# Kernel tuning notes

Hardware: AMD Instinct MI355X
Metric: run time of the kernel (lower is better)

The kernel has to match this reference:

```python
import jax, jax.numpy as jnp
import numpy as np

# ---- static config (matches init_kwargs) ----
B = 8            # batch_size (graphs)
N = 10000        # num_nodes per graph
NTOT = B * N     # total node rows (80000)
E = 320000       # edges (only over first N nodes, as in the original code)
D = 128          # input_dim == backbone_channels (shared conv forces equality)
H = 4            # heads
C = 128          # backbone_channels (per-head out dim, concat=False)
L = 3            # num_backbone_layers
K = 30           # sort-pool k
HID = 512        # mlp_hidden_dim
OUT = 2          # output_dim
EXPECTED = K * L * C * H + 1  # buggy mlp_input_dim from __init__ -> zero-pad
BN_EPS = 1e-5


def setup_inputs() -> dict:
    key = jax.random.key(0)
    ks = jax.random.split(key, 20)
    s = 1.0 / np.sqrt(D)
    inp = {
        "x": jax.random.normal(ks[0], (NTOT, D), dtype=jnp.float32),
        "edge_index": jax.random.randint(ks[1], (2, E), 0, N, dtype=jnp.int32),
        "age": jax.random.normal(ks[2], (B,), dtype=jnp.float32),
        # shared TransformerConv params (reused across all L layers)
        "Wq": jax.random.normal(ks[3], (D, H * C), dtype=jnp.float32) * s,
        "bq": jax.random.normal(ks[4], (H * C,), dtype=jnp.float32) * 0.02,
        "Wk": jax.random.normal(ks[5], (D, H * C), dtype=jnp.float32) * s,
        "bk": jax.random.normal(ks[6], (H * C,), dtype=jnp.float32) * 0.02,
        "Wv": jax.random.normal(ks[7], (D, H * C), dtype=jnp.float32) * s,
        "bv": jax.random.normal(ks[8], (H * C,), dtype=jnp.float32) * 0.02,
        "Wskip": jax.random.normal(ks[9], (D, C), dtype=jnp.float32) * s,
        "bskip": jax.random.normal(ks[10], (C,), dtype=jnp.float32) * 0.02,
        # per-layer BatchNorm (eval mode: running stats)
        "bn_gamma": 1.0 + 0.1 * jax.random.normal(ks[11], (L, C), dtype=jnp.float32),
        "bn_beta": 0.1 * jax.random.normal(ks[12], (L, C), dtype=jnp.float32),
        "bn_mean": 0.1 * jax.random.normal(ks[13], (L, C), dtype=jnp.float32),
        "bn_var": jax.random.uniform(ks[14], (L, C), dtype=jnp.float32, minval=0.5, maxval=1.5),
        # MLP head (2 layers: EXPECTED->HID, ReLU, HID->OUT)
        "W1": jax.random.normal(ks[15], (EXPECTED, HID), dtype=jnp.float32) * (1.0 / np.sqrt(EXPECTED)),
        "b1": jnp.zeros((HID,), dtype=jnp.float32),
        "W2": jax.random.normal(ks[16], (HID, OUT), dtype=jnp.float32) * (1.0 / np.sqrt(HID)),
        "b2": jnp.zeros((OUT,), dtype=jnp.float32),
    }
    return inp


def _transformer_conv(h, src, dst, Wq, bq, Wk, bk, Wv, bv, Wskip, bskip):
    # PyG TransformerConv, concat=False, root_weight=True, eval (no attn dropout)
    q = (h @ Wq + bq).reshape(NTOT, H, C)
    k = (h @ Wk + bk).reshape(NTOT, H, C)
    v = (h @ Wv + bv).reshape(NTOT, H, C)
    # per-edge attention logits [E, H]
    alpha = jnp.einsum("ehc,ehc->eh", q[dst], k[src]) / np.sqrt(C).astype(np.float32)
    # segment softmax over incoming edges of each target node
    m = jax.ops.segment_max(alpha, dst, num_segments=NTOT)          # [NTOT, H]
    e = jnp.exp(alpha - m[dst])
    denom = jax.ops.segment_sum(e, dst, num_segments=NTOT)          # [NTOT, H]
    a = e / (denom[dst] + 1e-16)                                    # [E, H]
    out = jax.ops.segment_sum(a[:, :, None] * v[src], dst, num_segments=NTOT)  # [NTOT,H,C]
    return out.mean(axis=1) + h @ Wskip + bskip                     # concat=False -> head mean


def reference(x, edge_index, age, Wq, bq, Wk, bk, Wv, bv, Wskip, bskip,
              bn_gamma, bn_beta, bn_mean, bn_var, W1, b1, W2, b2):
    src, dst = edge_index[0], edge_index[1]
    h = x
    feats = []
    for i in range(L):  # fixed small layer count; shared conv weights
        h = _transformer_conv(h, src, dst, Wq, bq, Wk, bk, Wv, bv, Wskip, bskip)
        h = (h - bn_mean[i]) * (bn_gamma[i] / jnp.sqrt(bn_var[i] + BN_EPS)) + bn_beta[i]
        h = jax.nn.relu(h)  # dropout: eval mode no-op
        feats.append(h)
    h = feats[-1]  # concat_input_graph=False
    # global_sort_pool: sort nodes per graph by last channel (desc), take top-k
    xr = h.reshape(B, N, C)
    idx = jnp.argsort(-xr[:, :, -1], axis=1)[:, :K]                 # [B, K]
    pooled = jnp.take_along_axis(xr, idx[:, :, None], axis=1)       # [B, K, C]
    z = pooled.reshape(B, K * C)
    z = jnp.concatenate([z, age.reshape(B, 1)], axis=1)             # [B, K*C+1]
    # zero-pad to the (mismatched) expected MLP input dim, as in the original
    z = jnp.concatenate([z, jnp.zeros((B, EXPECTED - z.shape[1]), dtype=z.dtype)], axis=1)
    z = jax.nn.relu(z @ W1 + b1)
    z = z @ W2 + b2
    return jax.nn.log_softmax(z, axis=-1)
```

## Files before the change

### kernel.cpp

```cpp
#include <hip/hip_runtime.h>
#include <cmath>


#define NN    10000
#define NTOT  80000
#define EE    320000
#define CH    128

__device__ __forceinline__ float rl_f(float v, int lane) {
    return __uint_as_float(__builtin_amdgcn_readlane(__float_as_uint(v), lane));
}

__global__ __launch_bounds__(256) void precompute_kernel(
    const float* __restrict__ Wq, const float* __restrict__ bq,
    const float* __restrict__ Wk, const float* __restrict__ Wv,
    const float* __restrict__ bv, const float* __restrict__ Wskip,
    const float* __restrict__ bskip,
    const float* __restrict__ bn_gamma, const float* __restrict__ bn_beta,
    const float* __restrict__ bn_mean, const float* __restrict__ bn_var,
    float* __restrict__ Bcat, float* __restrict__ biascat,
    float* __restrict__ Wcomb, float* __restrict__ bvbar,
    float* __restrict__ bnS, float* __restrict__ bnB)
{
    const float inv_sqrtC = 0.08838834764831845f;
    int idx = blockIdx.x * 256 + threadIdx.x;
    if (idx < 65536) {
        int c = idx >> 9;
        int o = idx & 511;
        int hbase = o & ~127;
        int j = o & 127;
        const float* wq = Wq + c * 512 + hbase;
        const float* wk = Wk + j * 512 + hbase;
        float s = 0.f;
        for (int cc = 0; cc < 128; cc++) s = fmaf(wq[cc], wk[cc], s);
        Bcat[c * 640 + o] = s * inv_sqrtC;
        return;
    }
    idx -= 65536;
    if (idx < 16384) {
        int c = idx >> 7, n = idx & 127;
        Bcat[c * 640 + 512 + n] = Wskip[c * 128 + n];
        return;
    }
    idx -= 16384;
    if (idx < 512) {
        int o = idx, hbase = o & ~127, j = o & 127;
        const float* wk = Wk + j * 512 + hbase;
        const float* bqp = bq + hbase;
        float s = 0.f;
        for (int cc = 0; cc < 128; cc++) s = fmaf(bqp[cc], wk[cc], s);
        biascat[o] = s * inv_sqrtC;
        return;
    }
    idx -= 512;
    if (idx < 128) {
        biascat[512 + idx] = bskip[idx];
        return;
    }
    idx -= 128;
    if (idx < 65536) {
        int k = idx >> 7;
        int n = idx & 127;
        int h = k >> 7, c = k & 127;
        Wcomb[k * 128 + n] = Wv[c * 512 + h * 128 + n] * 0.25f;
        return;
    }
    idx -= 65536;
    if (idx < 128) {
        float s = 0.f;
        for (int h = 0; h < 4; h++) s += bv[h * 128 + idx];
        bvbar[idx] = 0.25f * s;
        return;
    }
    idx -= 128;
    if (idx < 384) {
        float sc = bn_gamma[idx] / sqrtf(bn_var[idx] + 1e-5f);
        bnS[idx] = sc;
        bnB[idx] = bn_beta[idx] - bn_mean[idx] * sc;
        return;
    }
}

__global__ void count_kernel(const int* __restrict__ dst, int* __restrict__ deg) {
    int e = blockIdx.x * 256 + threadIdx.x;
    if (e < EE) atomicAdd(&deg[dst[e]], 1);
}

__global__ __launch_bounds__(1024) void scan_kernel(const int* __restrict__ deg,
                                                    int* __restrict__ rowstart) {
    __shared__ int part[1024];
    const int t = threadIdx.x;
    int loc[10];
    int s = 0;
    for (int i = 0; i < 10; i++) {
        int idx = t * 10 + i;
        int v = (idx < NN) ? deg[idx] : 0;
        loc[i] = s; s += v;
    }
    part[t] = s; __syncthreads();
    for (int d = 1; d < 1024; d <<= 1) {
        int v = (t >= d) ? part[t - d] : 0;
        __syncthreads();
        part[t] += v;
        __syncthreads();
    }
    int base = (t == 0) ? 0 : part[t - 1];
    for (int i = 0; i < 10; i++) {
        int idx = t * 10 + i;
        if (idx <= NN) rowstart[idx] = base + loc[i];
    }
}

__global__ void scatter_kernel(const int* __restrict__ src, const int* __restrict__ dst,
                               const int* __restrict__ rowstart, int* __restrict__ cursor,
                               int* __restrict__ csr_src) {
    int e = blockIdx.x * 256 + threadIdx.x;
    if (e < EE) {
        int d = dst[e];
        int p = atomicAdd(&cursor[d], 1);
        csr_src[rowstart[d] + p] = src[e];
    }
}

__global__ __launch_bounds__(256, 4) void skip_keys_kernel(
    const float* __restrict__ xup,
    const float* __restrict__ Wskip,
    const float* __restrict__ bskip,
    const float* __restrict__ bnS, const float* __restrict__ bnB,
    float* __restrict__ gkeys)
{
    __shared__ float rowb[64][132];
    __shared__ float sWc[128];
    const int t = threadIdx.x;
    const int l = t & 63;
    const int wv = __builtin_amdgcn_readfirstlane(t >> 6);
    const int colbase = wv * 32;
    const int r0 = blockIdx.x * 64;
    const int Mrem = min(64, (NTOT - NN) - r0);

    for (int f = t; f < 64 * 32; f += 256) {
        int row = f >> 5, c4 = (f & 31) * 4;
        float4 v = make_float4(0.f, 0.f, 0.f, 0.f);
        if (row < Mrem) v = *(const float4*)(xup + (size_t)(r0 + row) * CH + c4);
        *(float4*)&rowb[row][c4] = v;
    }
    if (t < 128) sWc[t] = Wskip[t * 128 + 127];
    __syncthreads();

    for (int layer = 0; layer < 2; layer++) {
        float acc[32];
        #pragma unroll
        for (int c = 0; c < 32; c++) acc[c] = 0.f;
        const float* Wb = Wskip + colbase;
        for (int kq = 0; kq < 32; kq++) {
            const float4 a4 = *(const float4*)&rowb[l][kq * 4];
            #pragma unroll
            for (int q = 0; q < 4; q++) {
                const float av = (q == 0) ? a4.x : (q == 1) ? a4.y
                               : (q == 2) ? a4.z : a4.w;
                const float* wr = Wb + (kq * 4 + q) * 128;
                #pragma unroll
                for (int c = 0; c < 32; c++)
                    acc[c] = fmaf(av, wr[c], acc[c]);
            }
        }
        __syncthreads();
        const float* bS = bnS + layer * 128;
        const float* bB = bnB + layer * 128;
        #pragma unroll
        for (int c4 = 0; c4 < 8; c4++) {
            float4 v;
            float* vp = &v.x;
            #pragma unroll
            for (int q = 0; q < 4; q++) {
                const int n = colbase + c4 * 4 + q;
                float xv = acc[c4 * 4 + q] + bskip[n];
                xv = fmaf(xv, bS[n], bB[n]);
                vp[q] = fmaxf(xv, 0.f);
            }
            *(float4*)&rowb[l][colbase + c4 * 4] = v;
        }
        __syncthreads();
    }
    if (t < Mrem) {
        float s = 0.f;
        for (int k = 0; k < 128; k++) s = fmaf(rowb[t][k], sWc[k], s);
        s += bskip[127];
        s = fmaf(s, bnS[2 * 128 + 127], bnB[2 * 128 + 127]);
        gkeys[NN + r0 + t] = fmaxf(s, 0.f);
    }
}

template<int BM, int BN, int TM, int TN, int MODE>
__global__ __launch_bounds__(256) void gemm_fp32(
    const float* __restrict__ A, int lda,
    const float* __restrict__ B, int ldb,
    const float* __restrict__ bias, const float* __restrict__ bias2,
    const int* __restrict__ deg,
    const float* __restrict__ Cold,
    const float* __restrict__ bnS, const float* __restrict__ bnB,
    float* __restrict__ C0, int ldc0,
    float* __restrict__ C1, int ldc1,
    int M, int K,
    float* __restrict__ keysOut)
{
    constexpr int BK = 16;
    __shared__ float As[BK][BM + 4];
    __shared__ float Bs[BK][BN + 4];
    const int t  = threadIdx.x;
    const int tx = t % (BN / TN);
    const int ty = t / (BN / TN);
    const int m0 = blockIdx.x * BM;
    const int n0 = blockIdx.y * BN;
    float acc[TM][TN];
    #pragma unroll
    for (int i = 0; i < TM; i++)
        #pragma unroll
        for (int j = 0; j < TN; j++) acc[i][j] = 0.f;

    for (int k0 = 0; k0 < K; k0 += BK) {
        #pragma unroll
        for (int f = t; f < BM * 4; f += 256) {
            int row = f >> 2, fc = f & 3;
            int gm = m0 + row;
            float4 v = make_float4(0.f, 0.f, 0.f, 0.f);
            if (gm < M) v = *(const float4*)(A + (size_t)gm * lda + k0 + fc * 4);
            As[fc * 4 + 0][row] = v.x;
            As[fc * 4 + 1][row] = v.y;
            As[fc * 4 + 2][row] = v.z;
            As[fc * 4 + 3][row] = v.w;
        }
        #pragma unroll
        for (int f = t; f < BK * (BN / 4); f += 256) {
            int kk = f / (BN / 4);
            int nn = (f % (BN / 4)) * 4;
            *(float4*)(&Bs[kk][nn]) = *(const float4*)(B + (size_t)(k0 + kk) * ldb + n0 + nn);
        }
        __syncthreads();
        #pragma unroll
        for (int kk = 0; kk < BK; kk++) {
            float af[TM], bf[TN];
            if constexpr (TM == 2) {
                float2 v = *(const float2*)&As[kk][ty * 2];
                af[0] = v.x; af[1] = v.y;
            } else {
                float4 v = *(const float4*)&As[kk][ty * 4];
                af[0] = v.x; af[1] = v.y; af[2] = v.z; af[3] = v.w;
            }
            if constexpr (TN == 4) {
                float4 v = *(const float4*)&Bs[kk][tx * 4];
                bf[0] = v.x; bf[1] = v.y; bf[2] = v.z; bf[3] = v.w;
            } else {
                float4 v = *(const float4*)&Bs[kk][tx * 4];
                float4 w = *(const float4*)&Bs[kk][BN / 2 + tx * 4];
                bf[0] = v.x; bf[1] = v.y; bf[2] = v.z; bf[3] = v.w;
                bf[4] = w.x; bf[5] = w.y; bf[6] = w.z; bf[7] = w.w;
            }
            #pragma unroll
            for (int i = 0; i < TM; i++)
                #pragma unroll
                for (int j = 0; j < TN; j++)
                    acc[i][j] = fmaf(af[i], bf[j], acc[i][j]);
        }
        __syncthreads();
    }
    #pragma unroll
    for (int i = 0; i < TM; i++) {
        const int gm = m0 + ty * TM + i;
        if (gm >= M) continue;
        const bool addB2 = (MODE == 4) ? (deg[gm] > 0) : false;
        #pragma unroll
        for (int h = 0; h < TN / 4; h++) {
            const int nb = n0 + ((TN == 8) ? h * (BN / 2) + tx * 4 : tx * TN + h * 4);
            float4 v;
            float* vp = &v.x;
            if (MODE == 4) {
                const float4 old = *(const float4*)(Cold + (size_t)gm * ldc1 + nb);
                const float* op = &old.x;
                #pragma unroll
                for (int q = 0; q < 4; q++) {
                    const int n = nb + q;
                    float x = acc[i][h * 4 + q] + op[q];
                    if (addB2) x += bias2[n];
                    x = fmaf(x, bnS[n], bnB[n]);
                    vp[q] = fmaxf(x, 0.f);
                }
                *(float4*)(C0 + (size_t)gm * ldc0 + nb) = v;
                if (keysOut != nullptr && nb == 124) keysOut[gm] = v.w;
            } else {
                #pragma unroll
                for (int q = 0; q < 4; q++)
                    vp[q] = acc[i][h * 4 + q] + bias[nb + q];
                if (nb < 512)
                    *(float4*)(C0 + (size_t)gm * ldc0 + nb) = v;
                else
                    *(float4*)(C1 + (size_t)gm * ldc1 + nb - 512) = v;
            }
        }
    }
}

__global__ __launch_bounds__(256) void attn_kernel(
    const float* __restrict__ h,
    const float* __restrict__ u,
    float* __restrict__ g,
    const int* __restrict__ rowstart,
    const int* __restrict__ csr_src)
{
    __shared__ float h_lds[128 * 65];
    __shared__ __align__(16) float palpha[4 * 64 * 4];
    __shared__ __align__(16) float wT[64 * 4];
    __shared__ __align__(16) float scale_lds[4];
    __shared__ __align__(16) float s_lds[4];
    __shared__ __align__(16) float merge[128 * 4];
    __shared__ int src_lds[64];

    const int n  = blockIdx.x;
    const int t  = threadIdx.x;
    const int w  = t >> 6;
    const int l  = t & 63;
    const int c  = t & 127;
    const int jh = t >> 7;
    const int rs   = rowstart[n];
    const int degn = rowstart[n + 1] - rs;

    if (degn == 0) {
        g[(size_t)n * 512 + t] = 0.f;
        g[(size_t)n * 512 + 256 + t] = 0.f;
        return;
    }
    float u_reg0 = u[(size_t)n * 512 + ((l >> 5)) * 128 + 32 * w + (l & 31)];
    float u_reg1 = u[(size_t)n * 512 + ((l >> 5) + 2) * 128 + 32 * w + (l & 31)];

    float m_run = -INFINITY, s_run = 0.f;
    float4 acc4 = make_float4(0.f, 0.f, 0.f, 0.f);

    for (int base = 0; base < degn; base += 64) {
        const int len = min(64, degn - base);
        __syncthreads();
        if (t < len) src_lds[t] = csr_src[rs + base + t];
        __syncthreads();
        for (int f = t; f < len * 32; f += 256) {
            const int j = f >> 5, c4 = (f & 31) * 4;
            const float4 v = *(const float4*)(h + (size_t)src_lds[j] * CH + c4);
            h_lds[(c4 + 0) * 65 + j] = v.x;
            h_lds[(c4 + 1) * 65 + j] = v.y;
            h_lds[(c4 + 2) * 65 + j] = v.z;
            h_lds[(c4 + 3) * 65 + j] = v.w;
        }
        __syncthreads();
        {
            float p0 = 0.f, p1 = 0.f, p2 = 0.f, p3 = 0.f;
            #pragma unroll
            for (int dc = 0; dc < 32; dc++) {
                const float hv = h_lds[(32 * w + dc) * 65 + l];
                p0 = fmaf(rl_f(u_reg0, dc),      hv, p0);
                p1 = fmaf(rl_f(u_reg0, 32 + dc), hv, p1);
                p2 = fmaf(rl_f(u_reg1, dc),      hv, p2);
                p3 = fmaf(rl_f(u_reg1, 32 + dc), hv, p3);
            }
            palpha[(0 * 64 + l) * 4 + w] = p0;
            palpha[(1 * 64 + l) * 4 + w] = p1;
            palpha[(2 * 64 + l) * 4 + w] = p2;
            palpha[(3 * 64 + l) * 4 + w] = p3;
        }
        __syncthreads();
        {
            const float4 pa = *(const float4*)&palpha[(w * 64 + l) * 4];
            float alpha = (l < len) ? (pa.x + pa.y + pa.z + pa.w) : -INFINITY;
            float mx = alpha;
            #pragma unroll
            for (int d = 1; d < 64; d <<= 1) mx = fmaxf(mx, __shfl_xor(mx, d, 64));
            const float newm = fmaxf(m_run, mx);
            float e = (l < len) ? __expf(alpha - newm) : 0.f;
            float ss = e;
            #pragma unroll
            for (int d = 1; d < 64; d <<= 1) ss += __shfl_xor(ss, d, 64);
            const float sc = (m_run == -INFINITY) ? 0.f : __expf(m_run - newm);
            s_run = s_run * sc + ss;
            m_run = newm;
            wT[l * 4 + w] = e;
            if (l == 0) scale_lds[w] = sc;
        }
        __syncthreads();
        {
            const float4 scv = *(const float4*)scale_lds;
            acc4.x *= scv.x; acc4.y *= scv.y; acc4.z *= scv.z; acc4.w *= scv.w;
            const int j0 = jh * 32;
            const int j1 = min(len, j0 + 32);
            for (int j = j0; j < j1; j++) {
                const float hv = h_lds[c * 65 + j];
                const float4 wv = *(const float4*)&wT[j * 4];
                acc4.x = fmaf(wv.x, hv, acc4.x);
                acc4.y = fmaf(wv.y, hv, acc4.y);
                acc4.z = fmaf(wv.z, hv, acc4.z);
                acc4.w = fmaf(wv.w, hv, acc4.w);
            }
        }
    }
    if (l == 0) s_lds[w] = s_run;
    __syncthreads();
    if (jh == 1) *(float4*)&merge[c * 4] = acc4;
    __syncthreads();
    if (jh == 0) {
        const float4 o  = *(const float4*)&merge[c * 4];
        const float4 sv = *(const float4*)s_lds;
        g[(size_t)n * 512 + 0 * 128 + c] = (acc4.x + o.x) / (sv.x + 1e-16f);
        g[(size_t)n * 512 + 1 * 128 + c] = (acc4.y + o.y) / (sv.y + 1e-16f);
        g[(size_t)n * 512 + 2 * 128 + c] = (acc4.z + o.z) / (sv.z + 1e-16f);
        g[(size_t)n * 512 + 3 * 128 + c] = (acc4.w + o.w) / (sv.w + 1e-16f);
    }
}

__global__ __launch_bounds__(256) void radix_pool_kernel(
    const float* __restrict__ gkeys, const float* __restrict__ age,
    int* __restrict__ sel, float* __restrict__ z)
{
    __shared__ unsigned int keys[NN];
    __shared__ int hist[256];
    __shared__ int sbuf[256];
    __shared__ unsigned int sel_prefix;
    __shared__ int sel_need;
    __shared__ int gt_counter;
    __shared__ unsigned int cand_key[30];
    __shared__ int cand_idx[30];
    __shared__ int order[30];

    const int b = blockIdx.x;
    const int t = threadIdx.x;

    for (int i = t; i < NN; i += 256)
        keys[i] = __float_as_uint(gkeys[(size_t)b * NN + i]);
    if (t == 0) { sel_prefix = 0u; sel_need = 30; gt_counter = 0; }
    __syncthreads();

    for (int r = 3; r >= 0; r--) {
        hist[t] = 0;
        __syncthreads();
        const int shift = r * 8;
        const unsigned int pmask = (r == 3) ? 0u : (0xFFFFFFFFu << ((r + 1) * 8));
        const unsigned int pref = sel_prefix;
        const int need = sel_need;
        for (int i = t; i < NN; i += 256) {
            unsigned int k = keys[i];
            if ((k & pmask) == pref)
                atomicAdd(&hist[(k >> shift) & 255u], 1);
        }
        __syncthreads();
        sbuf[t] = hist[255 - t];
        __syncthreads();
        for (int d = 1; d < 256; d <<= 1) {
            int o = (t >= d) ? sbuf[t - d] : 0;
            __syncthreads();
            sbuf[t] += o;
            __syncthreads();
        }
        {
            const int v = t;
            const int ge = sbuf[255 - v];
            const int gt = ge - hist[v];
            if (gt < need && need <= ge) {
                sel_prefix = pref | ((unsigned int)v << shift);
                sel_need = need - gt;
            }
        }
        __syncthreads();
    }

    const unsigned int T = sel_prefix;
    const int need_eq = sel_need;
    const int n_gt = 30 - need_eq;

    for (int i = t; i < NN; i += 256) {
        unsigned int k = keys[i];
        if (k > T) {
            int p = atomicAdd(&gt_counter, 1);
            cand_key[p] = k; cand_idx[p] = i;
        }
    }
    {
        const int CHK = (NN + 255) / 256;
        const int i0 = t * CHK, i1 = min(NN, i0 + CHK);
        int local = 0;
        for (int i = i0; i < i1; i++) if (keys[i] == T) local++;
        sbuf[t] = local;
        __syncthreads();
        for (int d = 1; d < 256; d <<= 1) {
            int o = (t >= d) ? sbuf[t - d] : 0;
            __syncthreads();
            sbuf[t] += o;
            __syncthreads();
        }
        int rank = (t == 0) ? 0 : sbuf[t - 1];
        for (int i = i0; i < i1; i++) {
            if (keys[i] == T) {
                if (rank < need_eq) { cand_key[n_gt + rank] = T; cand_idx[n_gt + rank] = i; }
                rank++;
            }
        }
    }
    __syncthreads();
    if (t < 30) {
        const unsigned int mk = cand_key[t];
        const int mi = cand_idx[t];
        int rk = 0;
        for (int j = 0; j < 30; j++) {
            const unsigned int ok = cand_key[j];
            const int oi = cand_idx[j];
            if (ok > mk || (ok == mk && oi < mi)) rk++;
        }
        order[rk] = t;
    }
    __syncthreads();
    if (t < 30) sel[b * 30 + t] = cand_idx[order[t]];
    if (t == 0) z[(size_t)b * 3841 + 3840] = age[b];
}

__global__ __launch_bounds__(128) void gather_kernel(
    const float* __restrict__ h3,
    const float* __restrict__ x,
    const float* __restrict__ Wskip, const float* __restrict__ bskip,
    const float* __restrict__ bnS, const float* __restrict__ bnB,
    const int* __restrict__ sel, float* __restrict__ z)
{
    __shared__ float buf0[128], buf1[128];
    const int blk = blockIdx.x;
    const int b = blk / 30;
    const int kk = blk % 30;
    const int c = threadIdx.x;
    const int i = sel[b * 30 + kk];
    const size_t g = (size_t)b * NN + i;
    float v;
    if (b == 0) {
        v = h3[g * CH + c];
    } else {
        float* rd = buf0;
        float* wr = buf1;
        buf0[c] = x[g * CH + c];
        __syncthreads();
        float s = 0.f;
        for (int l = 0; l < 3; l++) {
            s = 0.f;
            for (int k = 0; k < 128; k++) s = fmaf(rd[k], Wskip[k * 128 + c], s);
            s += bskip[c];
            s = fmaf(s, bnS[l * 128 + c], bnB[l * 128 + c]);
            s = fmaxf(s, 0.f);
            if (l < 2) {
                wr[c] = s;
                __syncthreads();
                float* tmp = rd; rd = wr; wr = tmp;
            }
        }
        v = s;
    }
    z[(size_t)b * 3841 + kk * CH + c] = v;
}

__global__ __launch_bounds__(256) void mlp1_kernel(
    const float* __restrict__ z, const float* __restrict__ W1,
    float* __restrict__ zh)
{
    __shared__ float zs[256];
    const int b  = blockIdx.x >> 4;
    const int ic = blockIdx.x & 15;
    const int t  = threadIdx.x;
    const int i0 = ic * 241;
    const int i1 = min(3841, i0 + 241);
    float a0 = 0.f, a1 = 0.f;
    for (int cb = i0; cb < i1; cb += 256) {
        int cl = min(256, i1 - cb);
        __syncthreads();
        if (t < cl) zs[t] = z[(size_t)b * 3841 + cb + t];
        __syncthreads();
        #pragma unroll 4
        for (int q = 0; q < cl; q++) {
            float zv = zs[q];
            const float* wp = W1 + (size_t)(cb + q) * 512;
            a0 = fmaf(zv, wp[t], a0);
            a1 = fmaf(zv, wp[t + 256], a1);
        }
    }
    atomicAdd(&zh[(size_t)b * 512 + t], a0);
    atomicAdd(&zh[(size_t)b * 512 + t + 256], a1);
}

__global__ __launch_bounds__(256) void mlp2_kernel(
    const float* __restrict__ zh, const float* __restrict__ b1,
    const float* __restrict__ W2, const float* __restrict__ b2,
    float* __restrict__ out)
{
    __shared__ float r0[256], r1[256];
    const int b = blockIdx.x;
    const int t = threadIdx.x;
    float a0 = 0.f, a1 = 0.f;
    for (int j = t; j < 512; j += 256) {
        float v = fmaxf(zh[(size_t)b * 512 + j] + b1[j], 0.f);
        a0 = fmaf(v, W2[j * 2 + 0], a0);
        a1 = fmaf(v, W2[j * 2 + 1], a1);
    }
    r0[t] = a0; r1[t] = a1; __syncthreads();
    for (int s = 128; s > 0; s >>= 1) {
        if (t < s) { r0[t] += r0[t + s]; r1[t] += r1[t + s]; }
        __syncthreads();
    }
    if (t == 0) {
        float l0 = r0[0] + b2[0], l1 = r1[0] + b2[1];
        float m = fmaxf(l0, l1);
        float lse = m + logf(__expf(l0 - m) + __expf(l1 - m));
        out[b * 2 + 0] = l0 - lse;
        out[b * 2 + 1] = l1 - lse;
    }
}

extern "C" void kernel_launch(void* const* d_in, const int* in_sizes, int n_in,
                              void* d_out, int out_size, void* d_ws, size_t ws_size,
                              hipStream_t stream) {
    const float* x     = (const float*)d_in[0];
    const int*   ei    = (const int*)d_in[1];
    const float* age   = (const float*)d_in[2];
    const float* Wq    = (const float*)d_in[3];
    const float* bq    = (const float*)d_in[4];
    const float* Wk    = (const float*)d_in[5];
    const float* Wv    = (const float*)d_in[7];
    const float* bv    = (const float*)d_in[8];
    const float* Wskip = (const float*)d_in[9];
    const float* bskip = (const float*)d_in[10];
    const float* bn_g  = (const float*)d_in[11];
    const float* bn_b  = (const float*)d_in[12];
    const float* bn_m  = (const float*)d_in[13];
    const float* bn_v  = (const float*)d_in[14];
    const float* W1    = (const float*)d_in[15];
    const float* b1    = (const float*)d_in[16];
    const float* W2    = (const float*)d_in[17];
    const float* b2    = (const float*)d_in[18];

    float* ws = (float*)d_ws;
    float* h3      = ws;
    float* hlowA   = h3 + 10240000;
    float* hlowB   = hlowA + 1280000;
    float* u       = hlowB + 1280000;
    float* skipraw = u + 5120000;
    float* Bcat    = skipraw + 1280000;
    float* biascat = Bcat + 81920;
    float* Wcomb   = biascat + 640;
    float* bvbar   = Wcomb + 65536;
    float* bnS     = bvbar + 128;
    float* bnB     = bnS + 384;
    float* zbuf    = bnB + 384;
    float* zh      = zbuf + 30728;
    int* deg      = (int*)(zh + 4096);
    int* cursor   = deg + NN;
    int* rowstart = cursor + NN;
    int* csr_src  = rowstart + NN + 1;
    float* keysG  = (float*)(csr_src + EE);
    int* sel      = (int*)(keysG + NTOT);

    const int* srcI = ei;
    const int* dstI = ei + EE;

    hipMemsetAsync(deg, 0, sizeof(int) * (2 * NN), stream);
    hipMemsetAsync(zh, 0, sizeof(float) * 4096, stream);

    precompute_kernel<<<581, 256, 0, stream>>>(Wq, bq, Wk, Wv, bv, Wskip, bskip,
                                               bn_g, bn_b, bn_m, bn_v,
                                               Bcat, biascat, Wcomb, bvbar, bnS, bnB);
    count_kernel<<<1250, 256, 0, stream>>>(dstI, deg);
    scan_kernel<<<1, 1024, 0, stream>>>(deg, rowstart);
    scatter_kernel<<<1250, 256, 0, stream>>>(srcI, dstI, rowstart, cursor, csr_src);

    skip_keys_kernel<<<1094, 256, 0, stream>>>(x + (size_t)NN * CH, Wskip, bskip,
                                               bnS, bnB, keysG);

    const float* hcur = x;
    for (int l = 0; l < 3; l++) {
        float* dest = (l == 0) ? hlowA : (l == 1) ? hlowB : h3;
        gemm_fp32<64, 64, 4, 4, 0><<<dim3(157, 10), 256, 0, stream>>>(
            hcur, CH, Bcat, 640, biascat, nullptr, nullptr, nullptr,
            nullptr, nullptr, u, 512, skipraw, CH, NN, 128, nullptr);
        attn_kernel<<<NN, 256, 0, stream>>>(hcur, u, u, rowstart, csr_src);
        gemm_fp32<32, 64, 2, 4, 4><<<dim3(313, 2), 256, 0, stream>>>(
            u, 512, Wcomb, CH, nullptr, bvbar, deg, skipraw,
            bnS + l * 128, bnB + l * 128, dest, CH, nullptr, CH, NN, 512,
            (l == 2) ? keysG : nullptr);
        hcur = dest;
    }
    radix_pool_kernel<<<8, 256, 0, stream>>>(keysG, age, sel, zbuf);
    gather_kernel<<<240, 128, 0, stream>>>(h3, x, Wskip, bskip,
                                           bnS, bnB, sel, zbuf);
    mlp1_kernel<<<128, 256, 0, stream>>>(zbuf, W1, zh);
    mlp2_kernel<<<8, 256, 0, stream>>>(zh, b1, W2, b2, (float*)d_out);
}
```

Measured before the change: 617.6 us.

## Fuse skip projection GEMM into the output GEMM epilogue instead of precomputing

The first GEMM no longer computes the skip projection columns (grid shrinks from 10 to 8 column tiles), so the skipraw buffer is neither written nor re-read. The output GEMM instead runs a second K=128 loop over hcur and Wskip into a separate accumulator and adds bskip in the epilogue. This drops a global write and read of an NN×128 intermediate per layer, at the cost of extra registers and more work in the smaller output GEMM.

```diff
diff --git a/kernel.cpp b/kernel.cpp
--- a/kernel.cpp
+++ b/kernel.cpp
@@ -197,10 +197,10 @@
     const float* __restrict__ B, int ldb,
     const float* __restrict__ bias, const float* __restrict__ bias2,
     const int* __restrict__ deg,
-    const float* __restrict__ Cold,
+    const float* __restrict__ A2,
+    const float* __restrict__ B2,
     const float* __restrict__ bnS, const float* __restrict__ bnB,
     float* __restrict__ C0, int ldc0,
-    float* __restrict__ C1, int ldc1,
     int M, int K,
     float* __restrict__ keysOut)
 {
@@ -213,10 +213,11 @@
     const int m0 = blockIdx.x * BM;
     const int n0 = blockIdx.y * BN;
     float acc[TM][TN];
+    float acc2[TM][TN];
     #pragma unroll
     for (int i = 0; i < TM; i++)
         #pragma unroll
-        for (int j = 0; j < TN; j++) acc[i][j] = 0.f;
+        for (int j = 0; j < TN; j++) { acc[i][j] = 0.f; acc2[i][j] = 0.f; }
 
     for (int k0 = 0; k0 < K; k0 += BK) {
         #pragma unroll
@@ -264,6 +265,56 @@
         }
         __syncthreads();
     }
+
+    if constexpr (MODE == 4) {
+        for (int k0 = 0; k0 < 128; k0 += BK) {
+            #pragma unroll
+            for (int f = t; f < BM * 4; f += 256) {
+                int row = f >> 2, fc = f & 3;
+                int gm = m0 + row;
+                float4 v = make_float4(0.f, 0.f, 0.f, 0.f);
+                if (gm < M) v = *(const float4*)(A2 + (size_t)gm * 128 + k0 + fc * 4);
+                As[fc * 4 + 0][row] = v.x;
+                As[fc * 4 + 1][row] = v.y;
+                As[fc * 4 + 2][row] = v.z;
+                As[fc * 4 + 3][row] = v.w;
+            }
+            #pragma unroll
+            for (int f = t; f < BK * (BN / 4); f += 256) {
+                int kk = f / (BN / 4);
+                int nn = (f % (BN / 4)) * 4;
+                *(float4*)(&Bs[kk][nn]) = *(const float4*)(B2 + (size_t)(k0 + kk) * 128 + n0 + nn);
+            }
+            __syncthreads();
+            #pragma unroll
+            for (int kk = 0; kk < BK; kk++) {
+                float af[TM], bf[TN];
+                if constexpr (TM == 2) {
+                    float2 v = *(const float2*)&As[kk][ty * 2];
+                    af[0] = v.x; af[1] = v.y;
+                } else {
+                    float4 v = *(const float4*)&As[kk][ty * 4];
+                    af[0] = v.x; af[1] = v.y; af[2] = v.z; af[3] = v.w;
+                }
+                if constexpr (TN == 4) {
+                    float4 v = *(const float4*)&Bs[kk][tx * 4];
+                    bf[0] = v.x; bf[1] = v.y; bf[2] = v.z; bf[3] = v.w;
+                } else {
+                    float4 v = *(const float4*)&Bs[kk][tx * 4];
+                    float4 w = *(const float4*)&Bs[kk][BN / 2 + tx * 4];
+                    bf[0] = v.x; bf[1] = v.y; bf[2] = v.z; bf[3] = v.w;
+                    bf[4] = w.x; bf[5] = w.y; bf[6] = w.z; bf[7] = w.w;
+                }
+                #pragma unroll
+                for (int i = 0; i < TM; i++)
+                    #pragma unroll
+                    for (int j = 0; j < TN; j++)
+                        acc2[i][j] = fmaf(af[i], bf[j], acc2[i][j]);
+            }
+            __syncthreads();
+        }
+    }
+
     #pragma unroll
     for (int i = 0; i < TM; i++) {
         const int gm = m0 + ty * TM + i;
@@ -275,12 +326,11 @@
             float4 v;
             float* vp = &v.x;
             if (MODE == 4) {
-                const float4 old = *(const float4*)(Cold + (size_t)gm * ldc1 + nb);
-                const float* op = &old.x;
                 #pragma unroll
                 for (int q = 0; q < 4; q++) {
                     const int n = nb + q;
-                    float x = acc[i][h * 4 + q] + op[q];
+                    const float opq = acc2[i][h * 4 + q] + bias[n];
+                    float x = acc[i][h * 4 + q] + opq;
                     if (addB2) x += bias2[n];
                     x = fmaf(x, bnS[n], bnB[n]);
                     vp[q] = fmaxf(x, 0.f);
@@ -291,10 +341,7 @@
                 #pragma unroll
                 for (int q = 0; q < 4; q++)
                     vp[q] = acc[i][h * 4 + q] + bias[nb + q];
-                if (nb < 512)
-                    *(float4*)(C0 + (size_t)gm * ldc0 + nb) = v;
-                else
-                    *(float4*)(C1 + (size_t)gm * ldc1 + nb - 512) = v;
+                *(float4*)(C0 + (size_t)gm * ldc0 + nb) = v;
             }
         }
     }
@@ -674,13 +721,16 @@
     const float* hcur = x;
     for (int l = 0; l < 3; l++) {
         float* dest = (l == 0) ? hlowA : (l == 1) ? hlowB : h3;
-        gemm_fp32<64, 64, 4, 4, 0><<<dim3(157, 10), 256, 0, stream>>>(
-            hcur, CH, Bcat, 640, biascat, nullptr, nullptr, nullptr,
-            nullptr, nullptr, u, 512, skipraw, CH, NN, 128, nullptr);
+        gemm_fp32<64, 64, 4, 4, 0><<<dim3(157, 8), 256, 0, stream>>>(
+            hcur, CH, Bcat, 640, biascat, nullptr, nullptr,
+            nullptr, nullptr, nullptr, nullptr,
+            u, 512, NN, 128, nullptr);
         attn_kernel<<<NN, 256, 0, stream>>>(hcur, u, u, rowstart, csr_src);
         gemm_fp32<32, 64, 2, 4, 4><<<dim3(313, 2), 256, 0, stream>>>(
-            u, 512, Wcomb, CH, nullptr, bvbar, deg, skipraw,
-            bnS + l * 128, bnB + l * 128, dest, CH, nullptr, CH, NN, 512,
+            u, 512, Wcomb, CH, bskip, bvbar, deg,
+            hcur, Wskip,
+            bnS + l * 128, bnB + l * 128,
+            dest, CH, NN, 512,
             (l == 2) ? keysG : nullptr);
         hcur = dest;
     }
```

Result: no change. 628.0 us (+1.7%).
